# Performance work log

Hardware: AMD Instinct MI355X
Metric: run time of the kernel (lower is better)

## Reference

```python
import jax, jax.numpy as jnp
import numpy as np

N, E, R, D = 50000, 640000, 200, 128  # nodes, edges, relations, feat dim (in_feat==out_feat)
EPS = 1e-5  # LayerNorm eps
NEG_SLOPE = 0.01  # F.leaky_relu default

def _xavier(k, shape):
    gain = np.sqrt(2.0)  # calculate_gain('relu')
    std = gain * np.sqrt(2.0 / (shape[0] + shape[1]))
    a = np.sqrt(3.0) * std
    return jax.random.uniform(k, shape, jnp.float32, -a, a)

def setup_inputs() -> dict:
    key = jax.random.key(0)
    ks = jax.random.split(key, 10)
    return {
        "node": jax.random.normal(ks[0], (N, D), jnp.float32),
        "rel": jax.random.normal(ks[1], (R, D), jnp.float32),
        "norm": jax.random.uniform(ks[2], (N, 1), jnp.float32),
        "w_triplet": _xavier(ks[3], (3 * D, D)),
        "w_quad": _xavier(ks[4], (D, D)),
        "loop_weight": _xavier(ks[5], (D, D)),
        "evolve_loop_weight": _xavier(ks[6], (D, D)),
        "src": jax.random.randint(ks[7], (E,), 0, N),
        "dst": jax.random.randint(ks[8], (E,), 0, N),
        "etype": jax.random.randint(ks[9], (E,), 0, R),
    }

def reference(node, rel, norm, w_triplet, w_quad, loop_weight, evolve_loop_weight, src, dst, etype):
    # triplet = cat([h_src, rel_emb, h_dst], 1) @ w_triplet, computed blockwise
    # to avoid materializing the [E, 3D] concat.
    W_s, W_r, W_d = w_triplet[:D], w_triplet[D:2 * D], w_triplet[2 * D:]
    triplet = node[src] @ W_s + rel[etype] @ W_r + node[dst] @ W_d  # [E, D]
    # 'fre' not in edata -> sro_fre is zeros; a_triplet = triplet @ w_quad
    a = jax.nn.leaky_relu(triplet @ w_quad, negative_slope=NEG_SLOPE)  # [E, D]
    # edge_softmax: softmax over incoming edges per destination node, per feature
    a_max = jax.ops.segment_max(a, dst, num_segments=N)
    a_max = jnp.where(jnp.isfinite(a_max), a_max, 0.0)  # empty segments -> -inf
    ex = jnp.exp(a - a_max[dst])
    denom = jax.ops.segment_sum(ex, dst, num_segments=N)
    att = ex / denom[dst]
    # weighted scatter-sum aggregation, then apply_func: h * norm
    h = jax.ops.segment_sum(att * triplet, dst, num_segments=N) * norm  # [N, D]
    # self-loop: evolve_loop_weight for in-degree-0 nodes, loop_weight otherwise
    indeg = jax.ops.segment_sum(jnp.ones((E,), jnp.float32), dst, num_segments=N)
    loop = jnp.where((indeg > 0)[:, None], node @ loop_weight, node @ evolve_loop_weight)
    out = h + loop
    # LayerNorm(elementwise_affine=False)
    mu = jnp.mean(out, axis=-1, keepdims=True)
    var = jnp.var(out, axis=-1, keepdims=True)
    return (out - mu) * jax.lax.rsqrt(var + EPS)
```

## Files before the change

kernel.cpp:

```cpp
#include <hip/hip_runtime.h>
#include <hip/hip_bf16.h>

#define D 128
#define LOG2E 1.4426950408889634f

typedef __attribute__((ext_vector_type(8))) short bf16x8;
typedef __attribute__((ext_vector_type(4))) float f32x4;
typedef __attribute__((ext_vector_type(2))) float f32x2;
typedef __attribute__((ext_vector_type(2))) unsigned u32x2;
typedef __attribute__((ext_vector_type(4))) unsigned u32x4;

__device__ __forceinline__ unsigned short f2bf_bits(float f) {
    union { __hip_bfloat16 h; unsigned short u; } c;
    c.h = __float2bfloat16(f);
    return c.u;
}
__device__ __forceinline__ float bfbits2f(unsigned short u) {
    return __uint_as_float(((unsigned)u) << 16);
}
__device__ __forceinline__ float ldf(const void* p, size_t i, int f32) {
    return f32 ? ((const float*)p)[i] : bfbits2f(((const unsigned short*)p)[i]);
}
__device__ __forceinline__ f32x2 unpk2(unsigned u) {
    f32x2 r;
    r.x = __uint_as_float(u << 16);
    r.y = __uint_as_float(u & 0xFFFF0000u);
    return r;
}
__device__ __forceinline__ f32x2 shx32(f32x2 v) {
    f32x2 r;
    r.x = __shfl_xor(v.x, 32);
    r.y = __shfl_xor(v.y, 32);
    return r;
}
__device__ __forceinline__ f32x2 pk_add(f32x2 a, f32x2 b) {
    f32x2 d;
    asm("v_pk_add_f32 %0, %1, %2" : "=v"(d) : "v"(a), "v"(b));
    return d;
}
__device__ __forceinline__ f32x2 pk_mul(f32x2 a, f32x2 b) {
    f32x2 d;
    asm("v_pk_mul_f32 %0, %1, %2" : "=v"(d) : "v"(a), "v"(b));
    return d;
}
__device__ __forceinline__ f32x2 pk_fma(f32x2 a, f32x2 b, f32x2 c) {
    f32x2 d;
    asm("v_pk_fma_f32 %0, %1, %2, %3" : "=v"(d) : "v"(a), "v"(b), "v"(c));
    return d;
}
__device__ __forceinline__ float fexp2(float x) {
    float r;
    asm("v_exp_f32 %0, %1" : "=v"(r) : "v"(x));
    return r;
}

__device__ __forceinline__ size_t fragIdx(int row, int k) {
    int f16 = ((row >> 4) * 4 + (k >> 5)) * 64 + ((k >> 3) & 3) * 16 + (row & 15);
    return (size_t)f16 * 8 + (k & 7);
}

__global__ __launch_bounds__(256) void prep_kernel(
    const void* __restrict__ node, const void* __restrict__ wtrip,
    const void* __restrict__ wquad, const void* __restrict__ loopW,
    const void* __restrict__ evoW, unsigned short* __restrict__ wT,
    int* __restrict__ cnt, int* __restrict__ rank,
    const int* __restrict__ dst, int* __restrict__ flag, int E) {
    __shared__ int sflag;
    int tid = threadIdx.x;
    int bad = 0;
    if (tid < 64) {
        for (int j = 0; j < 4; j++) {
            float v = bfbits2f(((const unsigned short*)node)[tid + 64 * j]);
            if (!(fabsf(v) < 1e4f)) bad = 1;
        }
    }
    unsigned long long m = __ballot(bad);
    if (tid == 0) sflag = (m != 0ull) ? 1 : 0;
    __syncthreads();
    int f32 = sflag;
    int bx = blockIdx.x;
    if (bx == 0 && tid == 0) *flag = f32;

    if (bx < 192) {
        int unit = bx * 2 + (tid >> 7);
        int k = unit & 127, mjob = unit >> 7;
        int t = tid & 127;
        float acc = 0.f;
        for (int j = 0; j < D; j++)
            acc += ldf(wtrip, (size_t)mjob * D * D + (size_t)k * D + j, f32) *
                   ldf(wquad, (size_t)j * D + t, f32);
        const int jmap0 = (mjob == 0) ? 0 : (mjob == 1 ? 6 : 2);
        wT[(size_t)jmap0 * D * D + fragIdx(t, k)] = f2bf_bits(acc);
    } else if (bx < 272) {
        int u = bx - 192;
        int jr = u >> 4, seg = u & 15;
        const void* srcp; size_t base; int j;
        switch (jr) {
            case 0: srcp = wtrip; base = 0;             j = 1; break;
            case 1: srcp = wtrip; base = 2 * D * D;     j = 3; break;
            case 2: srcp = loopW; base = 0;             j = 4; break;
            case 3: srcp = evoW;  base = 0;             j = 5; break;
            default: srcp = wtrip; base = (size_t)D * D; j = 7; break;
        }
        for (int c = tid; c < 1024; c += 256) {
            int idx = seg * 1024 + c;
            int n = idx >> 7, k = idx & 127;
            unsigned short b = f32 ? f2bf_bits(((const float*)srcp)[base + (size_t)k * D + n])
                                   : ((const unsigned short*)srcp)[base + (size_t)k * D + n];
            wT[(size_t)j * D * D + fragIdx(n, k)] = b;
        }
    } else {
        int e = (bx - 272) * 256 + tid;
        if (e < E) rank[e] = atomicAdd(&cnt[dst[e]], 1);
    }
}

__global__ void scan_block(const int* __restrict__ cnt, int* __restrict__ offs,
                           int* __restrict__ part, int N) {
    __shared__ int sh[256];
    int tid = threadIdx.x;
    int i = blockIdx.x * 256 + tid;
    int v = (i < N) ? cnt[i] : 0;
    sh[tid] = v;
    __syncthreads();
    for (int o = 1; o < 256; o <<= 1) {
        int t = (tid >= o) ? sh[tid - o] : 0;
        __syncthreads();
        sh[tid] += t;
        __syncthreads();
    }
    if (i < N) offs[i] = sh[tid] - v;
    if (tid == 255) part[blockIdx.x] = sh[255];
}

__global__ void scan_fix(int* __restrict__ offs, const int* __restrict__ part,
                         int N, int E) {
    __shared__ int sh[256];
    int tid = threadIdx.x, b = blockIdx.x;
    sh[tid] = (tid < b) ? part[tid] : 0;
    __syncthreads();
    for (int o = 128; o; o >>= 1) {
        if (tid < o) sh[tid] += sh[tid + o];
        __syncthreads();
    }
    int carry = sh[0];
    int i = b * 256 + tid;
    if (i < N) offs[i] += carry;
    if (b == 0 && tid == 0) offs[N] = E;
}

__global__ __launch_bounds__(512) void gemm_kernel(
    const void* __restrict__ node, const void* __restrict__ rel,
    const unsigned short* __restrict__ wT, const int* __restrict__ cnt,
    unsigned* __restrict__ nodeST, unsigned* __restrict__ nodeDT,
    unsigned* __restrict__ relRT, unsigned* __restrict__ loopSel,
    const int* __restrict__ flag, int N, int R, int nodeBlocks,
    const int* __restrict__ src, const int* __restrict__ dst,
    const int* __restrict__ et, const int* __restrict__ offs,
    const int* __restrict__ rank, u32x2* __restrict__ ePack, int E) {
    __shared__ __align__(16) unsigned short Wt[2][D * D];

    int bx = blockIdx.x, by = blockIdx.y;
    int tid = threadIdx.y * 64 + threadIdx.x;
    int isRel = 0, jp;
    if (bx >= nodeBlocks) {
        if (by == 1) {
            int e = (bx - nodeBlocks) * 512 + tid;
            if (e < E) {
                int d = dst[e];
                u32x2 pk;
                pk.x = ((unsigned)src[e]) << 9;
                pk.y = ((unsigned)et[e]) << 9;
                ePack[offs[d] + rank[e]] = pk;
            }
            return;
        }
        if (by != 0 || bx - nodeBlocks >= (R + 127) / 128) return;
        isRel = 1;
        jp = 3;
    } else {
        jp = by;
    }

    int f32 = *flag;
    int rows = isRel ? R : N;
    int row0 = (isRel ? bx - nodeBlocks : bx) * 128;
    const void* A = isRel ? rel : node;

    int lane = threadIdx.x, wv = threadIdx.y;
    int l16 = lane & 15, quad = lane >> 4;
    int ar = row0 + wv * 16 + l16;
    int ar_c = ar < rows ? ar : rows - 1;

    int qIdx, tIdx;
    unsigned* O = nullptr;
    switch (jp) {
        case 0: qIdx = 0; tIdx = 1; O = nodeST; break;
        case 1: qIdx = 2; tIdx = 3; O = nodeDT; break;
        case 2: qIdx = 4; tIdx = 5; break;
        default: qIdx = 6; tIdx = 7; O = relRT; break;
    }

    const unsigned short* gQ = wT + (size_t)qIdx * D * D;
    const unsigned short* gT = wT + (size_t)tIdx * D * D;

    bf16x8 wq[4], wt[4];
#pragma unroll
    for (int i = 0; i < 4; i++)
        wq[i] = *(const bf16x8*)(gQ + (size_t)(tid + i * 512) * 8);
#pragma unroll
    for (int i = 0; i < 4; i++)
        wt[i] = *(const bf16x8*)(gT + (size_t)(tid + i * 512) * 8);

    bf16x8 af[4];
#pragma unroll
    for (int kk = 0; kk < 4; kk++) {
        int k = kk * 32 + quad * 8;
        if (f32) {
            const float* Af = (const float*)A + (size_t)ar_c * D + k;
            float4 x0 = *(const float4*)(Af);
            float4 x1 = *(const float4*)(Af + 4);
            af[kk][0] = (short)f2bf_bits(x0.x);
            af[kk][1] = (short)f2bf_bits(x0.y);
            af[kk][2] = (short)f2bf_bits(x0.z);
            af[kk][3] = (short)f2bf_bits(x0.w);
            af[kk][4] = (short)f2bf_bits(x1.x);
            af[kk][5] = (short)f2bf_bits(x1.y);
            af[kk][6] = (short)f2bf_bits(x1.z);
            af[kk][7] = (short)f2bf_bits(x1.w);
        } else {
            af[kk] = *(const bf16x8*)((const unsigned short*)A + (size_t)ar_c * D + k);
        }
    }

#pragma unroll
    for (int i = 0; i < 4; i++)
        *(bf16x8*)(&Wt[0][(size_t)(tid + i * 512) * 8]) = wq[i];
#pragma unroll
    for (int i = 0; i < 4; i++)
        *(bf16x8*)(&Wt[1][(size_t)(tid + i * 512) * 8]) = wt[i];

    f32x4 accQ[8], accT[8];
#pragma unroll
    for (int i = 0; i < 8; i++) {
        accQ[i] = (f32x4){0.f, 0.f, 0.f, 0.f};
        accT[i] = (f32x4){0.f, 0.f, 0.f, 0.f};
    }

    __syncthreads();

#pragma unroll
    for (int nt = 0; nt < 8; nt++) {
#pragma unroll
        for (int kk = 0; kk < 4; kk++) {
            bf16x8 bq = *(const bf16x8*)(&Wt[0][(size_t)((nt * 4 + kk) * 64 + lane) * 8]);
            accQ[nt] = __builtin_amdgcn_mfma_f32_16x16x32_bf16(af[kk], bq, accQ[nt], 0, 0, 0);
        }
    }
#pragma unroll
    for (int nt = 0; nt < 8; nt++) {
#pragma unroll
        for (int kk = 0; kk < 4; kk++) {
            bf16x8 bt = *(const bf16x8*)(&Wt[1][(size_t)((nt * 4 + kk) * 64 + lane) * 8]);
            accT[nt] = __builtin_amdgcn_mfma_f32_16x16x32_bf16(af[kk], bt, accT[nt], 0, 0, 0);
        }
    }

    int cr0 = row0 + wv * 16 + quad * 4;
    int odd = l16 & 1;
    if (jp != 2) {
#pragma unroll
        for (int r = 0; r < 4; r++) {
            int cr = cr0 + r;
#pragma unroll
            for (int nt = 0; nt < 8; nt++) {
                float vQ = accQ[nt][r] * LOG2E;
                float vT = accT[nt][r];
                float oQ = __shfl_xor(vQ, 1);
                float oT = __shfl_xor(vT, 1);
                unsigned w;
                if (!odd) w = (unsigned)f2bf_bits(vQ) | ((unsigned)f2bf_bits(oQ) << 16);
                else      w = (unsigned)f2bf_bits(oT) | ((unsigned)f2bf_bits(vT) << 16);
                if (cr < rows) O[(size_t)cr * 128 + nt * 16 + l16] = w;
            }
        }
    } else {
#pragma unroll
        for (int r = 0; r < 4; r++) {
            int cr = cr0 + r;
            int deg = (cr < rows) ? cnt[cr] : 0;
#pragma unroll
            for (int nt = 0; nt < 8; nt++) {
                float vL = accQ[nt][r], vE = accT[nt][r];
                float oL = __shfl_xor(vL, 1);
                float oE = __shfl_xor(vE, 1);
                unsigned wl, we;
                if (!odd) {
                    wl = (unsigned)f2bf_bits(vL) | ((unsigned)f2bf_bits(oL) << 16);
                    we = (unsigned)f2bf_bits(vE) | ((unsigned)f2bf_bits(oE) << 16);
                } else {
                    wl = (unsigned)f2bf_bits(oL) | ((unsigned)f2bf_bits(vL) << 16);
                    we = (unsigned)f2bf_bits(oE) | ((unsigned)f2bf_bits(vE) << 16);
                }
                if (cr < rows && !odd)
                    loopSel[(size_t)cr * 64 + nt * 8 + (l16 >> 1)] = (deg > 0) ? wl : we;
            }
        }
    }
}

__global__ __launch_bounds__(256) void agg_kernel(
    const int* __restrict__ offs, const u32x2* __restrict__ ePack,
    const unsigned* __restrict__ ST, const unsigned* __restrict__ RT,
    const unsigned* __restrict__ DT, const unsigned* __restrict__ loopSel,
    const void* __restrict__ normv, void* __restrict__ out,
    const int* __restrict__ flag, int N) {
    int n = blockIdx.x * 4 + threadIdx.y;
    if (n >= N) return;
    int f32 = *flag;
    int lane = threadIdx.x;
    int half = lane >> 5, sl = lane & 31;
    int start = offs[n], end = offs[n + 1];
    int deg = end - start;

    u32x4 ud = *(const u32x4*)(DT + (size_t)n * 128 + sl * 4);
    f32x2 qd01 = unpk2(ud.x), td01 = unpk2(ud.y);
    f32x2 qd23 = unpk2(ud.z), td23 = unpk2(ud.w);
    u32x2 ul = *(const u32x2*)(loopSel + (size_t)n * 64 + sl * 2);
    f32x2 acc01 = unpk2(ul.x), acc23 = unpk2(ul.y);

    const char* STb = (const char*)ST;
    const char* RTb = (const char*)RT;
    unsigned laneoff = (unsigned)(sl * 16);

    f32x2 den01 = {0.f, 0.f}, den23 = {0.f, 0.f};
    f32x2 h01 = {0.f, 0.f}, h23 = {0.f, 0.f};
    const f32x2 ns2 = {0.01f, 0.01f};

#define GLOAD(PK, US, UR)                                                   \
    u32x4 US = *(const u32x4*)(STb + (size_t)((PK).x + laneoff));           \
    u32x4 UR = *(const u32x4*)(RTb + (size_t)((PK).y + laneoff));

#define EMATH(US, UR)                                                       \
    {                                                                       \
        f32x2 q01 = pk_add(pk_add(unpk2(US.x), unpk2(UR.x)), qd01);         \
        f32x2 q23 = pk_add(pk_add(unpk2(US.z), unpk2(UR.z)), qd23);         \
        f32x2 s01 = pk_mul(q01, ns2);                                       \
        f32x2 s23 = pk_mul(q23, ns2);                                       \
        f32x2 ex01, ex23;                                                   \
        ex01.x = fexp2(fmaxf(q01.x, s01.x));                                \
        ex01.y = fexp2(fmaxf(q01.y, s01.y));                                \
        ex23.x = fexp2(fmaxf(q23.x, s23.x));                                \
        ex23.y = fexp2(fmaxf(q23.y, s23.y));                                \
        den01 = pk_add(den01, ex01); den23 = pk_add(den23, ex23);           \
        f32x2 t01 = pk_add(pk_add(unpk2(US.y), unpk2(UR.y)), td01);         \
        f32x2 t23 = pk_add(pk_add(unpk2(US.w), unpk2(UR.w)), td23);         \
        h01 = pk_fma(ex01, t01, h01);                                       \
        h23 = pk_fma(ex23, t23, h23);                                       \
    }

#define EMATHV(US, UR, VM)                                                  \
    {                                                                       \
        f32x2 q01 = pk_add(pk_add(unpk2(US.x), unpk2(UR.x)), qd01);         \
        f32x2 q23 = pk_add(pk_add(unpk2(US.z), unpk2(UR.z)), qd23);         \
        f32x2 s01 = pk_mul(q01, ns2);                                       \
        f32x2 s23 = pk_mul(q23, ns2);                                       \
        f32x2 ex01, ex23;                                                   \
        ex01.x = fexp2(fmaxf(q01.x, s01.x)) * (VM);                         \
        ex01.y = fexp2(fmaxf(q01.y, s01.y)) * (VM);                         \
        ex23.x = fexp2(fmaxf(q23.x, s23.x)) * (VM);                         \
        ex23.y = fexp2(fmaxf(q23.y, s23.y)) * (VM);                         \
        den01 = pk_add(den01, ex01); den23 = pk_add(den23, ex23);           \
        f32x2 t01 = pk_add(pk_add(unpk2(US.y), unpk2(UR.y)), td01);         \
        f32x2 t23 = pk_add(pk_add(unpk2(US.w), unpk2(UR.w)), td23);         \
        h01 = pk_fma(ex01, t01, h01);                                       \
        h23 = pk_fma(ex23, t23, h23);                                       \
    }

    int e = start;
    for (; e + 3 < end; e += 4) {
        u32x2 pA = ePack[e + half];
        u32x2 pB = ePack[e + 2 + half];
        GLOAD(pA, usA, urA)
        GLOAD(pB, usB, urB)
        EMATH(usA, urA)
        EMATH(usB, urB)
    }
    for (; e < end; e += 2) {
        int eh = e + half;
        int valid = eh < end;
        u32x2 pT = ePack[valid ? eh : end - 1];
        GLOAD(pT, usT, urT)
        EMATHV(usT, urT, valid ? 1.0f : 0.0f)
    }
#undef GLOAD
#undef EMATH
#undef EMATHV

    den01 = pk_add(den01, shx32(den01)); den23 = pk_add(den23, shx32(den23));
    h01 = pk_add(h01, shx32(h01));       h23 = pk_add(h23, shx32(h23));

    f32x2 x01, x23;
    if (deg > 0) {
        float nrm = ldf(normv, n, f32);
        x01 = h01 / den01 * nrm + acc01;
        x23 = h23 / den23 * nrm + acc23;
    } else {
        x01 = acc01;
        x23 = acc23;
    }

    float s = (x01.x + x01.y) + (x23.x + x23.y);
    float ss = (x01.x * x01.x + x01.y * x01.y) + (x23.x * x23.x + x23.y * x23.y);
#pragma unroll
    for (int o = 16; o; o >>= 1) {
        s += __shfl_xor(s, o);
        ss += __shfl_xor(ss, o);
    }
    float mu = s * (1.f / 128.f);
    float var = ss * (1.f / 128.f) - mu * mu;
    float rstd = rsqrtf(var + 1e-5f);
    f32x2 y01 = (x01 - mu) * rstd;
    f32x2 y23 = (x23 - mu) * rstd;

    if (half == 0) {
        if (f32) {
            float4 o4 = make_float4(y01.x, y01.y, y23.x, y23.y);
            ((float4*)out)[(size_t)n * 32 + sl] = o4;
        } else {
            u32x2 ow;
            ow.x = (unsigned)f2bf_bits(y01.x) | ((unsigned)f2bf_bits(y01.y) << 16);
            ow.y = (unsigned)f2bf_bits(y23.x) | ((unsigned)f2bf_bits(y23.y) << 16);
            *(u32x2*)((unsigned*)out + (size_t)n * 64 + sl * 2) = ow;
        }
    }
}

extern "C" void kernel_launch(void* const* d_in, const int* in_sizes, int n_in,
                              void* d_out, int out_size, void* d_ws, size_t ws_size,
                              hipStream_t stream) {
    const void* node = d_in[0];
    const void* rel = d_in[1];
    const void* normv = d_in[2];
    const void* wtrip = d_in[3];
    const void* wquad = d_in[4];
    const void* loopW = d_in[5];
    const void* evoW = d_in[6];
    const int* src = (const int*)d_in[7];
    const int* dst = (const int*)d_in[8];
    const int* et = (const int*)d_in[9];

    int N = in_sizes[0] / D;
    int R = in_sizes[1] / D;
    int E = in_sizes[7];
    int nb = (N + 255) / 256;
    int nodeBlocks = (N + 127) / 128;
    int relBlocks = (R + 127) / 128;
    int scatBlocks = (E + 511) / 512;

    char* p = (char*)d_ws;
    auto alloc = [&](size_t bytes) -> void* {
        void* r = (void*)p;
        p += (bytes + 255) & ~(size_t)255;
        return r;
    };
    unsigned* nodeST = (unsigned*)alloc((size_t)N * 128 * 4);
    unsigned* nodeDT = (unsigned*)alloc((size_t)N * 128 * 4);
    unsigned* relRT = (unsigned*)alloc((size_t)R * 128 * 4);
    unsigned* loopSel = (unsigned*)alloc((size_t)N * 64 * 4);
    unsigned short* wT = (unsigned short*)alloc((size_t)8 * D * D * 2);
    int* cnt = (int*)alloc((size_t)N * 4);
    int* offs = (int*)alloc((size_t)(N + 1) * 4);
    int* part = (int*)alloc((size_t)(nb + 1) * 4);
    int* rank = (int*)alloc((size_t)E * 4);
    u32x2* ePack = (u32x2*)alloc((size_t)E * 8);
    int* flag = (int*)alloc(4);

    hipMemsetAsync(cnt, 0, (size_t)N * 4, stream);
    prep_kernel<<<272 + (E + 255) / 256, 256, 0, stream>>>(
        node, wtrip, wquad, loopW, evoW, wT, cnt, rank, dst, flag, E);
    scan_block<<<nb, 256, 0, stream>>>(cnt, offs, part, N);
    scan_fix<<<nb, 256, 0, stream>>>(offs, part, N, E);
    int xext = nodeBlocks + (scatBlocks > relBlocks ? scatBlocks : relBlocks);
    gemm_kernel<<<dim3(xext, 3), dim3(64, 8), 0, stream>>>(
        node, rel, wT, cnt, nodeST, nodeDT, relRT, loopSel, flag, N, R, nodeBlocks,
        src, dst, et, offs, rank, ePack, E);
    agg_kernel<<<(N + 3) / 4, dim3(64, 4), 0, stream>>>(
        offs, ePack, nodeST, relRT, nodeDT, loopSel, normv, d_out, flag, N);
}
```

Baseline: 224.9 us.

## Fuse count, scan and scan-fix into prep kernel with software grid barriers

Folds the counter memset, per-destination counting, block scan and carry fix into the first nb blocks of the prep kernel. These blocks synchronise through atomic grid barriers, which removes two kernel launches and one memset from the stream. The barriers assume all nb scan blocks are co-resident (about 196 blocks, which is plausible on this GPU), otherwise the kernel deadlocks. Edge counting now runs on only nb blocks in a strided loop instead of one thread per edge, which could lower atomic throughput.

```diff
diff --git a/kernel.cpp b/kernel.cpp
--- a/kernel.cpp
+++ b/kernel.cpp
@@ -59,14 +59,62 @@
     return (size_t)f16 * 8 + (k & 7);
 }
 
+__device__ __forceinline__ void gridbar(int* bar, int idx, int nblk) {
+    __syncthreads();
+    if (threadIdx.x == 0) {
+        __threadfence();
+        atomicAdd(&bar[idx], 1);
+        while (atomicAdd(&bar[idx], 0) < nblk)
+            __builtin_amdgcn_s_sleep(2);
+        __threadfence();
+    }
+    __syncthreads();
+}
+
 __global__ __launch_bounds__(256) void prep_kernel(
     const void* __restrict__ node, const void* __restrict__ wtrip,
     const void* __restrict__ wquad, const void* __restrict__ loopW,
     const void* __restrict__ evoW, unsigned short* __restrict__ wT,
-    int* __restrict__ cnt, int* __restrict__ rank,
-    const int* __restrict__ dst, int* __restrict__ flag, int E) {
+    int* __restrict__ cnt, int* __restrict__ offs, int* __restrict__ part,
+    int* __restrict__ rank, const int* __restrict__ dst,
+    int* __restrict__ flag, int* __restrict__ bar, int E, int N, int nbScan) {
+    int tid = threadIdx.x;
+    int bx = blockIdx.x;
+
+    if (bx < nbScan) {
+        __shared__ int sh[256];
+        int i0 = bx * 256 + tid;
+        if (i0 < N) atomicExch(&cnt[i0], 0);
+        gridbar(bar, 0, nbScan);
+        for (int e = bx * 256 + tid; e < E; e += nbScan * 256)
+            rank[e] = atomicAdd(&cnt[dst[e]], 1);
+        gridbar(bar, 1, nbScan);
+        int v = (i0 < N) ? atomicAdd(&cnt[i0], 0) : 0;
+        sh[tid] = v;
+        __syncthreads();
+        for (int o = 1; o < 256; o <<= 1) {
+            int t = (tid >= o) ? sh[tid - o] : 0;
+            __syncthreads();
+            sh[tid] += t;
+            __syncthreads();
+        }
+        int myexcl = sh[tid] - v;
+        if (tid == 255) atomicExch(&part[bx], sh[255]);
+        gridbar(bar, 2, nbScan);
+        sh[tid] = (tid < bx) ? atomicAdd(&part[tid], 0) : 0;
+        __syncthreads();
+        for (int o = 128; o; o >>= 1) {
+            if (tid < o) sh[tid] += sh[tid + o];
+            __syncthreads();
+        }
+        int carry = sh[0];
+        if (i0 < N) offs[i0] = myexcl + carry;
+        if (bx == 0 && tid == 0) offs[N] = E;
+        return;
+    }
+
+    int wbx = bx - nbScan;
     __shared__ int sflag;
-    int tid = threadIdx.x;
     int bad = 0;
     if (tid < 64) {
         for (int j = 0; j < 4; j++) {
@@ -78,11 +126,10 @@
     if (tid == 0) sflag = (m != 0ull) ? 1 : 0;
     __syncthreads();
     int f32 = sflag;
-    int bx = blockIdx.x;
-    if (bx == 0 && tid == 0) *flag = f32;
-
-    if (bx < 192) {
-        int unit = bx * 2 + (tid >> 7);
+    if (wbx == 0 && tid == 0) *flag = f32;
+
+    if (wbx < 192) {
+        int unit = wbx * 2 + (tid >> 7);
         int k = unit & 127, mjob = unit >> 7;
         int t = tid & 127;
         float acc = 0.f;
@@ -91,8 +138,8 @@
                    ldf(wquad, (size_t)j * D + t, f32);
         const int jmap0 = (mjob == 0) ? 0 : (mjob == 1 ? 6 : 2);
         wT[(size_t)jmap0 * D * D + fragIdx(t, k)] = f2bf_bits(acc);
-    } else if (bx < 272) {
-        int u = bx - 192;
+    } else {
+        int u = wbx - 192;
         int jr = u >> 4, seg = u & 15;
         const void* srcp; size_t base; int j;
         switch (jr) {
@@ -109,44 +156,7 @@
                                    : ((const unsigned short*)srcp)[base + (size_t)k * D + n];
             wT[(size_t)j * D * D + fragIdx(n, k)] = b;
         }
-    } else {
-        int e = (bx - 272) * 256 + tid;
-        if (e < E) rank[e] = atomicAdd(&cnt[dst[e]], 1);
-    }
-}
-
-__global__ void scan_block(const int* __restrict__ cnt, int* __restrict__ offs,
-                           int* __restrict__ part, int N) {
-    __shared__ int sh[256];
-    int tid = threadIdx.x;
-    int i = blockIdx.x * 256 + tid;
-    int v = (i < N) ? cnt[i] : 0;
-    sh[tid] = v;
-    __syncthreads();
-    for (int o = 1; o < 256; o <<= 1) {
-        int t = (tid >= o) ? sh[tid - o] : 0;
-        __syncthreads();
-        sh[tid] += t;
-        __syncthreads();
-    }
-    if (i < N) offs[i] = sh[tid] - v;
-    if (tid == 255) part[blockIdx.x] = sh[255];
-}
-
-__global__ void scan_fix(int* __restrict__ offs, const int* __restrict__ part,
-                         int N, int E) {
-    __shared__ int sh[256];
-    int tid = threadIdx.x, b = blockIdx.x;
-    sh[tid] = (tid < b) ? part[tid] : 0;
-    __syncthreads();
-    for (int o = 128; o; o >>= 1) {
-        if (tid < o) sh[tid] += sh[tid + o];
-        __syncthreads();
-    }
-    int carry = sh[0];
-    int i = b * 256 + tid;
-    if (i < N) offs[i] += carry;
-    if (b == 0 && tid == 0) offs[N] = E;
+    }
 }
 
 __global__ __launch_bounds__(512) void gemm_kernel(
@@ -475,12 +485,12 @@
     int* rank = (int*)alloc((size_t)E * 4);
     u32x2* ePack = (u32x2*)alloc((size_t)E * 8);
     int* flag = (int*)alloc(4);
-
-    hipMemsetAsync(cnt, 0, (size_t)N * 4, stream);
-    prep_kernel<<<272 + (E + 255) / 256, 256, 0, stream>>>(
-        node, wtrip, wquad, loopW, evoW, wT, cnt, rank, dst, flag, E);
-    scan_block<<<nb, 256, 0, stream>>>(cnt, offs, part, N);
-    scan_fix<<<nb, 256, 0, stream>>>(offs, part, N, E);
+    int* bar = (int*)alloc(64);
+
+    hipMemsetAsync(bar, 0, 64, stream);
+    prep_kernel<<<nb + 272, 256, 0, stream>>>(
+        node, wtrip, wquad, loopW, evoW, wT, cnt, offs, part, rank, dst,
+        flag, bar, E, N, nb);
     int xext = nodeBlocks + (scatBlocks > relBlocks ? scatBlocks : relBlocks);
     gemm_kernel<<<dim3(xext, 3), dim3(64, 8), 0, stream>>>(
         node, rel, wT, cnt, nodeST, nodeDT, relRT, loopSel, flag, N, R, nodeBlocks,
```

New measurement: 254.2 us. 1.13x slower.
